# Performance work log

Measured on AMD Instinct MI355X. Metric: run time of the kernel, lower is better.

The kernel has to match this reference:

```python
import jax, jax.numpy as jnp
import numpy as np

T, B, F, H, C = 512, 64, 256, 1024, 257

def setup_inputs() -> dict:
    key = jax.random.key(0)
    ks = jax.random.split(key, 16)
    s_in = 1.0 / np.sqrt(F)
    s_h = 1.0 / np.sqrt(H)
    inp = {
        'x': jax.random.normal(ks[0], (T, B, F), dtype=jnp.float32),
        'wfx_w': jax.random.uniform(ks[1], (H, F), jnp.float32, -s_in, s_in),
        'wfx_b': jax.random.uniform(ks[2], (H,), jnp.float32, -s_in, s_in),
        'wix_w': jax.random.uniform(ks[3], (H, F), jnp.float32, -s_in, s_in),
        'wix_b': jax.random.uniform(ks[4], (H,), jnp.float32, -s_in, s_in),
        'wox_w': jax.random.uniform(ks[5], (H, F), jnp.float32, -s_in, s_in),
        'wox_b': jax.random.uniform(ks[6], (H,), jnp.float32, -s_in, s_in),
        'wcx_w': jax.random.uniform(ks[7], (H, F), jnp.float32, -s_in, s_in),
        'wcx_b': jax.random.uniform(ks[8], (H,), jnp.float32, -s_in, s_in),
        'wfh_w': jax.random.uniform(ks[9], (H, H), jnp.float32, -s_h, s_h),
        'wih_w': jax.random.uniform(ks[10], (H, H), jnp.float32, -s_h, s_h),
        'woh_w': jax.random.uniform(ks[11], (H, H), jnp.float32, -s_h, s_h),
        'wch_w': jax.random.uniform(ks[12], (H, H), jnp.float32, -s_h, s_h),
        'fco_w': jax.random.uniform(ks[13], (C, H), jnp.float32, -s_h, s_h),
        'fco_b': jax.random.uniform(ks[14], (C,), jnp.float32, -s_h, s_h),
    }
    return inp


def reference(x, wfx_w, wfx_b, wix_w, wix_b, wox_w, wox_b, wcx_w, wcx_b,
              wfh_w, wih_w, woh_w, wch_w, fco_w, fco_b):
    # Precompute input-projection gates for all timesteps: [T, B, H] each.
    gf = jnp.einsum('tbf,hf->tbh', x, wfx_w) + wfx_b
    gi = jnp.einsum('tbf,hf->tbh', x, wix_w) + wix_b
    go = jnp.einsum('tbf,hf->tbh', x, wox_w) + wox_b
    gc = jnp.einsum('tbf,hf->tbh', x, wcx_w) + wcx_b
    gates_x = jnp.stack([gf, gi, go, gc], axis=1)  # [T, 4, B, H]

    # Stack recurrent weights for a single per-step GEMM: [4H, H].
    Wh = jnp.concatenate([wfh_w, wih_w, woh_w, wch_w], axis=0)
    Hd = wfh_w.shape[0]

    def step(carry, gx):
        h, c = carry
        rec = (h @ Wh.T).reshape(h.shape[0], 4, Hd).transpose(1, 0, 2)  # [4, B, H]
        z = gx + rec
        ft = jax.nn.sigmoid(z[0])
        it = jax.nn.sigmoid(z[1])
        ot = jax.nn.sigmoid(z[2])
        at = z[3]
        c = it * jnp.tanh(at) + ft * c
        h = ot * jnp.tanh(c)
        return (h, c), h

    B_ = x.shape[1]
    h0 = jnp.zeros((B_, Hd), dtype=x.dtype)
    (_, _), hs = jax.lax.scan(step, (h0, h0), gates_x)  # hs: [T, B, H]
    out = jnp.einsum('tbh,ch->tbc', hs, fco_w) + fco_b  # [T, B, C]
    return out
```

## Files before the change

### kernel.cpp

```cpp
#include <hip/hip_runtime.h>

#define T_STEPS 512
#define BATCH 64
#define FDIM 256
#define HDIM 1024
#define CDIM 257

typedef __attribute__((ext_vector_type(8))) short short8;
typedef __attribute__((ext_vector_type(4))) short short4_t;
typedef __attribute__((ext_vector_type(4))) float float4_t;
typedef __attribute__((ext_vector_type(2))) int int2_t;

__device__ __forceinline__ short f2bf(float f) {
  unsigned u = __builtin_bit_cast(unsigned, f);
  unsigned r = (u + 0x7fffu + ((u >> 16) & 1u)) >> 16;
  return (short)(r & 0xffffu);
}

__device__ __forceinline__ float sigmoid_f(float x) {
  return 1.0f / (1.0f + __expf(-x));
}
__device__ __forceinline__ float tanh_f(float x) {
  float s = __expf(-2.0f * fabsf(x));
  float t = (1.0f - s) / (1.0f + s);
  return (x < 0.0f) ? -t : t;
}

__device__ __forceinline__ void load_h_frags(const short* base, short8 (&bh)[8]) {
  float4_t r0, r1, r2, r3, r4, r5, r6, r7;
  asm volatile(
    "global_load_dwordx4 %0, %8, off sc0 sc1\n\t"
    "global_load_dwordx4 %1, %8, off offset:64 sc0 sc1\n\t"
    "global_load_dwordx4 %2, %8, off offset:128 sc0 sc1\n\t"
    "global_load_dwordx4 %3, %8, off offset:192 sc0 sc1\n\t"
    "global_load_dwordx4 %4, %8, off offset:256 sc0 sc1\n\t"
    "global_load_dwordx4 %5, %8, off offset:320 sc0 sc1\n\t"
    "global_load_dwordx4 %6, %8, off offset:384 sc0 sc1\n\t"
    "global_load_dwordx4 %7, %8, off offset:448 sc0 sc1\n\t"
    "s_waitcnt vmcnt(0)"
    : "=&v"(r0), "=&v"(r1), "=&v"(r2), "=&v"(r3),
      "=&v"(r4), "=&v"(r5), "=&v"(r6), "=&v"(r7)
    : "v"(base)
    : "memory");
  bh[0] = __builtin_bit_cast(short8, r0);
  bh[1] = __builtin_bit_cast(short8, r1);
  bh[2] = __builtin_bit_cast(short8, r2);
  bh[3] = __builtin_bit_cast(short8, r3);
  bh[4] = __builtin_bit_cast(short8, r4);
  bh[5] = __builtin_bit_cast(short8, r5);
  bh[6] = __builtin_bit_cast(short8, r6);
  bh[7] = __builtin_bit_cast(short8, r7);
}

__global__ void prep_kernel(const float* __restrict__ fco_w,
                            short* __restrict__ fcob,
                            short* __restrict__ hbuf,
                            unsigned* __restrict__ flg)
{
  const int tid = blockIdx.x * 256 + threadIdx.x;
  {
    const int idx = tid * 4;
    const int c = idx >> 10, k = idx & 1023;
    short4_t o;
    if (c < CDIM) {
      const float4_t f = *(const float4_t*)(fco_w + c * HDIM + k);
      o[0] = f2bf(f[0]); o[1] = f2bf(f[1]); o[2] = f2bf(f[2]); o[3] = f2bf(f[3]);
    } else {
      o[0] = 0; o[1] = 0; o[2] = 0; o[3] = 0;
    }
    *(short4_t*)(fcob + idx) = o;
  }
  if (tid < 16384) {
    short8 z = (short8){0,0,0,0,0,0,0,0};
    *(short8*)(hbuf + tid * 8) = z;
  }
  if (tid < 4096) flg[tid] = 0;
}

__global__ __launch_bounds__(256, 1) void lstm_kernel(
    const float* __restrict__ x,
    const float* __restrict__ wfx, const float* __restrict__ wix,
    const float* __restrict__ wox, const float* __restrict__ wcx,
    const float* __restrict__ bfx, const float* __restrict__ bix,
    const float* __restrict__ box, const float* __restrict__ bcx,
    const float* __restrict__ wfh, const float* __restrict__ wih,
    const float* __restrict__ woh, const float* __restrict__ wch,
    short* __restrict__ hs, short* __restrict__ hbuf,
    unsigned* __restrict__ flg)
{
  const int tid  = threadIdx.x;
  const int lane = tid & 63;
  const int w    = tid >> 6;
  const int quad = lane >> 4;
  const int lm   = lane & 15;
  const int cg   = blockIdx.x & 63;
  const int bq   = blockIdx.x >> 6;

  __shared__ float zbuf[2][16 * 320];

  const float* Wh[4] = {wfh, wih, woh, wch};
  const float* Wx[4] = {wfx, wix, wox, wcx};
  const float* Bx[4] = {bfx, bix, box, bcx};

  short8 wr[4][8];
  short8 wxf[4][2];
#pragma unroll
  for (int g = 0; g < 4; ++g) {
    const float* rw = Wh[g] + (cg * 16 + lm) * HDIM;
#pragma unroll
    for (int ktl = 0; ktl < 8; ++ktl) {
      const float* pk = rw + (w * 8 + ktl) * 32 + quad * 8;
      short8 a;
#pragma unroll
      for (int j = 0; j < 8; ++j) a[j] = f2bf(pk[j]);
      wr[g][ktl] = a;
    }
    const float* rx = Wx[g] + (cg * 16 + lm) * FDIM;
#pragma unroll
    for (int ktl = 0; ktl < 2; ++ktl) {
      const float* pk = rx + (w * 2 + ktl) * 32 + quad * 8;
      short8 a;
#pragma unroll
      for (int j = 0; j < 8; ++j) a[j] = f2bf(pk[j]);
      wxf[g][ktl] = a;
    }
  }

  float4_t biasv[4];
  float cst[4] = {0.f, 0.f, 0.f, 0.f};
  {
    const int i4 = lane >> 4;
#pragma unroll
    for (int g = 0; g < 4; ++g) {
#pragma unroll
      for (int r = 0; r < 4; ++r)
        biasv[g][r] = Bx[g][cg * 16 + i4 * 4 + r];
    }
  }

  unsigned* myf   = flg + ((bq * 4 + w) * 16 + lm) * 16;
  unsigned* prodf = flg + ((bq * 4 + (cg >> 4)) * 16 + (cg & 15)) * 16;

  for (int t = 0; t < T_STEPS; ++t) {
    const int p = t & 1;

    float4_t xf[2][2];
    {
      const float* xb = x + ((t * BATCH) + bq * 16 + lm) * FDIM;
#pragma unroll
      for (int i = 0; i < 2; ++i) {
        const float* pk = xb + (w * 2 + i) * 32 + quad * 8;
        xf[i][0] = *(const float4_t*)(pk);
        xf[i][1] = *(const float4_t*)(pk + 4);
      }
    }
    short8 bx[2];
#pragma unroll
    for (int i = 0; i < 2; ++i) {
      short8 a;
      a[0] = f2bf(xf[i][0][0]); a[1] = f2bf(xf[i][0][1]);
      a[2] = f2bf(xf[i][0][2]); a[3] = f2bf(xf[i][0][3]);
      a[4] = f2bf(xf[i][1][0]); a[5] = f2bf(xf[i][1][1]);
      a[6] = f2bf(xf[i][1][2]); a[7] = f2bf(xf[i][1][3]);
      bx[i] = a;
    }
    float4_t acc[4];
#pragma unroll
    for (int g = 0; g < 4; ++g) acc[g] = (float4_t){0.f, 0.f, 0.f, 0.f};
#pragma unroll
    for (int i = 0; i < 2; ++i) {
#pragma unroll
      for (int g = 0; g < 4; ++g)
        acc[g] = __builtin_amdgcn_mfma_f32_16x16x32_bf16(wxf[g][i], bx[i], acc[g], 0, 0, 0);
    }

    {
      const unsigned want = (unsigned)t;
      unsigned v;
      do {
        v = __hip_atomic_load(myf, __ATOMIC_RELAXED, __HIP_MEMORY_SCOPE_SYSTEM);
      } while (__all((int)(v >= want)) == 0);
    }

    short8 bh[8];
    load_h_frags(hbuf + (p ^ 1) * (BATCH * HDIM) + (bq * 16 + lm) * HDIM
                      + w * 256 + quad * 8, bh);

#pragma unroll
    for (int ktl = 0; ktl < 8; ++ktl) {
#pragma unroll
      for (int g = 0; g < 4; ++g)
        acc[g] = __builtin_amdgcn_mfma_f32_16x16x32_bf16(wr[g][ktl], bh[ktl], acc[g], 0, 0, 0);
    }

#pragma unroll
    for (int g = 0; g < 4; ++g)
      *(float4_t*)(&zbuf[p][(w * 4 + g) * 320 + lm * 20 + quad * 4]) = acc[g];

    __syncthreads();

    if (w == 0) {
      const int b = lane & 15, i4 = lane >> 4;
      const float* zb = &zbuf[p][b * 20 + i4 * 4];
      float4_t zs[4];
#pragma unroll
      for (int g = 0; g < 4; ++g) {
        float4_t v0 = *(const float4_t*)(zb + (0  + g) * 320);
        float4_t v1 = *(const float4_t*)(zb + (4  + g) * 320);
        float4_t v2 = *(const float4_t*)(zb + (8  + g) * 320);
        float4_t v3 = *(const float4_t*)(zb + (12 + g) * 320);
        zs[g] = (v0 + v1) + (v2 + v3) + biasv[g];
      }
      short4_t hv;
#pragma unroll
      for (int r = 0; r < 4; ++r) {
        float ff = sigmoid_f(zs[0][r]);
        float ii = sigmoid_f(zs[1][r]);
        float oo = sigmoid_f(zs[2][r]);
        float aa = tanh_f(zs[3][r]);
        float cn = ii * aa + ff * cst[r];
        cst[r] = cn;
        hv[r] = f2bf(oo * tanh_f(cn));
      }
      const int bg  = bq * 16 + b;
      const int col = cg * 16 + i4 * 4;
      {
        short* hp = hbuf + p * (BATCH * HDIM) + bg * HDIM + col;
        int2_t hv2 = __builtin_bit_cast(int2_t, hv);
        asm volatile("global_store_dwordx2 %0, %1, off sc0 sc1"
                     :: "v"(hp), "v"(hv2) : "memory");
      }
      *(short4_t*)(hs + ((t * BATCH) + bg) * HDIM + col) = hv;
      asm volatile("s_waitcnt vmcnt(0)" ::: "memory");
      if (lane == 0)
        __hip_atomic_store(prodf, (unsigned)(t + 1), __ATOMIC_RELAXED,
                           __HIP_MEMORY_SCOPE_SYSTEM);
    }
  }
}

__global__ __launch_bounds__(256, 2) void outproj_kernel(
    const short* __restrict__ hs,
    const short* __restrict__ fcob,
    const float* __restrict__ fco_bias,
    float* __restrict__ out)
{
  const int tid = threadIdx.x, lane = tid & 63, w = tid >> 6;
  const int quad = lane >> 4, lm = lane & 15;
  const int blk = blockIdx.x;

  short8 afr[32];
  const short* ar = hs + (blk * 64 + w * 16 + lm) * HDIM;
#pragma unroll
  for (int kt = 0; kt < 32; ++kt)
    afr[kt] = *(const short8*)(ar + kt * 32 + quad * 8);

  for (int nt = 0; nt < 17; ++nt) {
    float4_t a0 = (float4_t){0.f,0.f,0.f,0.f}, a1 = (float4_t){0.f,0.f,0.f,0.f};
    const short* br = fcob + (nt * 16 + lm) * HDIM + quad * 8;
#pragma unroll
    for (int kt = 0; kt < 32; kt += 2) {
      short8 b0 = *(const short8*)(br + kt * 32);
      a0 = __builtin_amdgcn_mfma_f32_16x16x32_bf16(afr[kt], b0, a0, 0, 0, 0);
      short8 b1 = *(const short8*)(br + (kt + 1) * 32);
      a1 = __builtin_amdgcn_mfma_f32_16x16x32_bf16(afr[kt + 1], b1, a1, 0, 0, 0);
    }
    const int c = nt * 16 + lm;
    if (c < CDIM) {
      const float bias = fco_bias[c];
      const int mb = blk * 64 + w * 16 + quad * 4;
#pragma unroll
      for (int r = 0; r < 4; ++r)
        out[(mb + r) * CDIM + c] = a0[r] + a1[r] + bias;
    }
  }
}

extern "C" void kernel_launch(void* const* d_in, const int* in_sizes, int n_in,
                              void* d_out, int out_size, void* d_ws, size_t ws_size,
                              hipStream_t stream) {
  (void)in_sizes; (void)n_in; (void)out_size; (void)ws_size;
  const float* x     = (const float*)d_in[0];
  const float* wfx_w = (const float*)d_in[1];
  const float* wfx_b = (const float*)d_in[2];
  const float* wix_w = (const float*)d_in[3];
  const float* wix_b = (const float*)d_in[4];
  const float* wox_w = (const float*)d_in[5];
  const float* wox_b = (const float*)d_in[6];
  const float* wcx_w = (const float*)d_in[7];
  const float* wcx_b = (const float*)d_in[8];
  const float* wfh_w = (const float*)d_in[9];
  const float* wih_w = (const float*)d_in[10];
  const float* woh_w = (const float*)d_in[11];
  const float* wch_w = (const float*)d_in[12];
  const float* fco_w = (const float*)d_in[13];
  const float* fco_b = (const float*)d_in[14];
  float* out = (float*)d_out;

  char* ws = (char*)d_ws;
  short*    hs   = (short*)(ws);
  short*    fcob = (short*)(ws + 67108864);
  short*    hbuf = (short*)(ws + 67108864 + 557056);
  unsigned* flg  = (unsigned*)(ws + 67108864 + 557056 + 262144);

  prep_kernel<<<272, 256, 0, stream>>>(fco_w, fcob, hbuf, flg);
  lstm_kernel<<<256, 256, 0, stream>>>(x,
                                       wfx_w, wix_w, wox_w, wcx_w,
                                       wfx_b, wix_b, wox_b, wcx_b,
                                       wfh_w, wih_w, woh_w, wch_w,
                                       hs, hbuf, flg);
  outproj_kernel<<<512, 256, 0, stream>>>(hs, fcob, fco_b, out);
}
```

Before: 2.186 ms.

## Merge LSTM column groups into 512-thread blocks with LDS-staged hidden state

Each workgroup now has 8 waves covering two 16-column tiles, so the grid drops from 256 to 128 blocks. Only wave 0 spin-waits on flags, then a block barrier releases the rest. The block loads the 16x1024 hidden-state slice once from global memory into swizzled LDS, and all waves read their MFMA fragments from there instead of each issuing its own global loads. Waves 3 and 7 run the gate epilogue, and the hs store is moved after the flag publish to shorten the critical path. In exchange each step adds extra block barriers and an LDS round trip, and the flag index layout is changed.

```diff
diff --git a/kernel.cpp b/kernel.cpp
--- a/kernel.cpp
+++ b/kernel.cpp
@@ -24,32 +24,6 @@
   float s = __expf(-2.0f * fabsf(x));
   float t = (1.0f - s) / (1.0f + s);
   return (x < 0.0f) ? -t : t;
-}
-
-__device__ __forceinline__ void load_h_frags(const short* base, short8 (&bh)[8]) {
-  float4_t r0, r1, r2, r3, r4, r5, r6, r7;
-  asm volatile(
-    "global_load_dwordx4 %0, %8, off sc0 sc1\n\t"
-    "global_load_dwordx4 %1, %8, off offset:64 sc0 sc1\n\t"
-    "global_load_dwordx4 %2, %8, off offset:128 sc0 sc1\n\t"
-    "global_load_dwordx4 %3, %8, off offset:192 sc0 sc1\n\t"
-    "global_load_dwordx4 %4, %8, off offset:256 sc0 sc1\n\t"
-    "global_load_dwordx4 %5, %8, off offset:320 sc0 sc1\n\t"
-    "global_load_dwordx4 %6, %8, off offset:384 sc0 sc1\n\t"
-    "global_load_dwordx4 %7, %8, off offset:448 sc0 sc1\n\t"
-    "s_waitcnt vmcnt(0)"
-    : "=&v"(r0), "=&v"(r1), "=&v"(r2), "=&v"(r3),
-      "=&v"(r4), "=&v"(r5), "=&v"(r6), "=&v"(r7)
-    : "v"(base)
-    : "memory");
-  bh[0] = __builtin_bit_cast(short8, r0);
-  bh[1] = __builtin_bit_cast(short8, r1);
-  bh[2] = __builtin_bit_cast(short8, r2);
-  bh[3] = __builtin_bit_cast(short8, r3);
-  bh[4] = __builtin_bit_cast(short8, r4);
-  bh[5] = __builtin_bit_cast(short8, r5);
-  bh[6] = __builtin_bit_cast(short8, r6);
-  bh[7] = __builtin_bit_cast(short8, r7);
 }
 
 __global__ void prep_kernel(const float* __restrict__ fco_w,
@@ -77,7 +51,7 @@
   if (tid < 4096) flg[tid] = 0;
 }
 
-__global__ __launch_bounds__(256, 1) void lstm_kernel(
+__global__ __launch_bounds__(512, 2) void lstm_kernel(
     const float* __restrict__ x,
     const float* __restrict__ wfx, const float* __restrict__ wix,
     const float* __restrict__ wox, const float* __restrict__ wcx,
@@ -88,15 +62,19 @@
     short* __restrict__ hs, short* __restrict__ hbuf,
     unsigned* __restrict__ flg)
 {
+  __shared__ float zbuf[2][16 * 320];
+  __shared__ short hlds[16 * 1024];
+
   const int tid  = threadIdx.x;
   const int lane = tid & 63;
   const int w    = tid >> 6;
+  const int kc   = w & 3;
+  const int tile = w >> 2;
   const int quad = lane >> 4;
   const int lm   = lane & 15;
-  const int cg   = blockIdx.x & 63;
-  const int bq   = blockIdx.x >> 6;
-
-  __shared__ float zbuf[2][16 * 320];
+  const int bq   = blockIdx.x & 3;
+  const int rank = blockIdx.x >> 2;
+  const int cb   = rank * 32 + tile * 16;
 
   const float* Wh[4] = {wfh, wih, woh, wch};
   const float* Wx[4] = {wfx, wix, wox, wcx};
@@ -106,19 +84,19 @@
   short8 wxf[4][2];
 #pragma unroll
   for (int g = 0; g < 4; ++g) {
-    const float* rw = Wh[g] + (cg * 16 + lm) * HDIM;
+    const float* rw = Wh[g] + (cb + lm) * HDIM;
 #pragma unroll
     for (int ktl = 0; ktl < 8; ++ktl) {
-      const float* pk = rw + (w * 8 + ktl) * 32 + quad * 8;
+      const float* pk = rw + (kc * 8 + ktl) * 32 + quad * 8;
       short8 a;
 #pragma unroll
       for (int j = 0; j < 8; ++j) a[j] = f2bf(pk[j]);
       wr[g][ktl] = a;
     }
-    const float* rx = Wx[g] + (cg * 16 + lm) * FDIM;
+    const float* rx = Wx[g] + (cb + lm) * FDIM;
 #pragma unroll
     for (int ktl = 0; ktl < 2; ++ktl) {
-      const float* pk = rx + (w * 2 + ktl) * 32 + quad * 8;
+      const float* pk = rx + (kc * 2 + ktl) * 32 + quad * 8;
       short8 a;
 #pragma unroll
       for (int j = 0; j < 8; ++j) a[j] = f2bf(pk[j]);
@@ -126,20 +104,20 @@
     }
   }
 
+  const int etile = (w == 7) ? 1 : 0;
+  const int eb = lane & 15, ei4 = lane >> 4;
+  const int ecol = rank * 32 + etile * 16 + ei4 * 4;
   float4_t biasv[4];
   float cst[4] = {0.f, 0.f, 0.f, 0.f};
-  {
-    const int i4 = lane >> 4;
-#pragma unroll
-    for (int g = 0; g < 4; ++g) {
-#pragma unroll
-      for (int r = 0; r < 4; ++r)
-        biasv[g][r] = Bx[g][cg * 16 + i4 * 4 + r];
-    }
-  }
-
-  unsigned* myf   = flg + ((bq * 4 + w) * 16 + lm) * 16;
-  unsigned* prodf = flg + ((bq * 4 + (cg >> 4)) * 16 + (cg & 15)) * 16;
+#pragma unroll
+  for (int g = 0; g < 4; ++g) {
+#pragma unroll
+    for (int r = 0; r < 4; ++r)
+      biasv[g][r] = Bx[g][ecol + r];
+  }
+
+  const unsigned* myf = flg + ((bq * 32 + (lane >> 1)) * 2 + (lane & 1)) * 16;
+  unsigned* pf        = flg + ((bq * 32 + rank) * 2 + etile) * 16;
 
   for (int t = 0; t < T_STEPS; ++t) {
     const int p = t & 1;
@@ -149,7 +127,7 @@
       const float* xb = x + ((t * BATCH) + bq * 16 + lm) * FDIM;
 #pragma unroll
       for (int i = 0; i < 2; ++i) {
-        const float* pk = xb + (w * 2 + i) * 32 + quad * 8;
+        const float* pk = xb + (kc * 2 + i) * 32 + quad * 8;
         xf[i][0] = *(const float4_t*)(pk);
         xf[i][1] = *(const float4_t*)(pk + 4);
       }
@@ -174,34 +152,67 @@
         acc[g] = __builtin_amdgcn_mfma_f32_16x16x32_bf16(wxf[g][i], bx[i], acc[g], 0, 0, 0);
     }
 
-    {
+    if (w == 0) {
       const unsigned want = (unsigned)t;
       unsigned v;
       do {
         v = __hip_atomic_load(myf, __ATOMIC_RELAXED, __HIP_MEMORY_SCOPE_SYSTEM);
       } while (__all((int)(v >= want)) == 0);
     }
-
-    short8 bh[8];
-    load_h_frags(hbuf + (p ^ 1) * (BATCH * HDIM) + (bq * 16 + lm) * HDIM
-                      + w * 256 + quad * 8, bh);
-
-#pragma unroll
-    for (int ktl = 0; ktl < 8; ++ktl) {
-#pragma unroll
-      for (int g = 0; g < 4; ++g)
-        acc[g] = __builtin_amdgcn_mfma_f32_16x16x32_bf16(wr[g][ktl], bh[ktl], acc[g], 0, 0, 0);
+    __syncthreads();
+
+    {
+      const int row = tid >> 5;
+      const int seg = tid & 31;
+      const short* src = hbuf + (p ^ 1) * (BATCH * HDIM)
+                              + (bq * 16 + row) * HDIM + seg * 32;
+      float4_t a0, a1, a2, a3;
+      asm volatile(
+        "global_load_dwordx4 %0, %4, off sc0 sc1\n\t"
+        "global_load_dwordx4 %1, %4, off offset:16 sc0 sc1\n\t"
+        "global_load_dwordx4 %2, %4, off offset:32 sc0 sc1\n\t"
+        "global_load_dwordx4 %3, %4, off offset:48 sc0 sc1\n\t"
+        "s_waitcnt vmcnt(0)"
+        : "=&v"(a0), "=&v"(a1), "=&v"(a2), "=&v"(a3)
+        : "v"(src)
+        : "memory");
+      const int bbase = row * 2048 + seg * 64;
+      const int sw = (row & 7) << 4;
+      *(short8*)((char*)hlds + ((bbase +  0) ^ sw)) = __builtin_bit_cast(short8, a0);
+      *(short8*)((char*)hlds + ((bbase + 16) ^ sw)) = __builtin_bit_cast(short8, a1);
+      *(short8*)((char*)hlds + ((bbase + 32) ^ sw)) = __builtin_bit_cast(short8, a2);
+      *(short8*)((char*)hlds + ((bbase + 48) ^ sw)) = __builtin_bit_cast(short8, a3);
+    }
+    __syncthreads();
+
+    {
+      const int hrow = lm * 2048;
+      const int hcol = kc * 512 + quad * 16;
+      const int hsw  = (lm & 7) << 4;
+#pragma unroll
+      for (int half = 0; half < 2; ++half) {
+        short8 b0 = *(const short8*)((const char*)hlds + ((hrow + hcol + (half*4+0)*64) ^ hsw));
+        short8 b1 = *(const short8*)((const char*)hlds + ((hrow + hcol + (half*4+1)*64) ^ hsw));
+        short8 b2 = *(const short8*)((const char*)hlds + ((hrow + hcol + (half*4+2)*64) ^ hsw));
+        short8 b3 = *(const short8*)((const char*)hlds + ((hrow + hcol + (half*4+3)*64) ^ hsw));
+#pragma unroll
+        for (int g = 0; g < 4; ++g) {
+          acc[g] = __builtin_amdgcn_mfma_f32_16x16x32_bf16(wr[g][half*4+0], b0, acc[g], 0, 0, 0);
+          acc[g] = __builtin_amdgcn_mfma_f32_16x16x32_bf16(wr[g][half*4+1], b1, acc[g], 0, 0, 0);
+          acc[g] = __builtin_amdgcn_mfma_f32_16x16x32_bf16(wr[g][half*4+2], b2, acc[g], 0, 0, 0);
+          acc[g] = __builtin_amdgcn_mfma_f32_16x16x32_bf16(wr[g][half*4+3], b3, acc[g], 0, 0, 0);
+        }
+      }
     }
 
 #pragma unroll
     for (int g = 0; g < 4; ++g)
-      *(float4_t*)(&zbuf[p][(w * 4 + g) * 320 + lm * 20 + quad * 4]) = acc[g];
+      *(float4_t*)(&zbuf[tile][(kc * 4 + g) * 320 + lm * 20 + quad * 4]) = acc[g];
 
     __syncthreads();
 
-    if (w == 0) {
-      const int b = lane & 15, i4 = lane >> 4;
-      const float* zb = &zbuf[p][b * 20 + i4 * 4];
+    if (w == 3 || w == 7) {
+      const float* zb = &zbuf[etile][eb * 20 + ei4 * 4];
       float4_t zs[4];
 #pragma unroll
       for (int g = 0; g < 4; ++g) {
@@ -222,19 +233,18 @@
         cst[r] = cn;
         hv[r] = f2bf(oo * tanh_f(cn));
       }
-      const int bg  = bq * 16 + b;
-      const int col = cg * 16 + i4 * 4;
+      const int bg = bq * 16 + eb;
       {
-        short* hp = hbuf + p * (BATCH * HDIM) + bg * HDIM + col;
+        short* hp = hbuf + p * (BATCH * HDIM) + bg * HDIM + ecol;
         int2_t hv2 = __builtin_bit_cast(int2_t, hv);
         asm volatile("global_store_dwordx2 %0, %1, off sc0 sc1"
                      :: "v"(hp), "v"(hv2) : "memory");
       }
-      *(short4_t*)(hs + ((t * BATCH) + bg) * HDIM + col) = hv;
       asm volatile("s_waitcnt vmcnt(0)" ::: "memory");
       if (lane == 0)
-        __hip_atomic_store(prodf, (unsigned)(t + 1), __ATOMIC_RELAXED,
+        __hip_atomic_store(pf, (unsigned)(t + 1), __ATOMIC_RELAXED,
                            __HIP_MEMORY_SCOPE_SYSTEM);
+      *(short4_t*)(hs + ((t * BATCH) + bg) * HDIM + ecol) = hv;
     }
   }
 }
@@ -304,7 +314,7 @@
   unsigned* flg  = (unsigned*)(ws + 67108864 + 557056 + 262144);
 
   prep_kernel<<<272, 256, 0, stream>>>(fco_w, fcob, hbuf, flg);
-  lstm_kernel<<<256, 256, 0, stream>>>(x,
+  lstm_kernel<<<128, 512, 0, stream>>>(x,
                                        wfx_w, wix_w, wox_w, wcx_w,
                                        wfx_b, wix_b, wox_b, wcx_b,
                                        wfh_w, wih_w, woh_w, wch_w,
```

New measurement: 2.592 ms. 18.6% more time.
